# Kernel tuning notes

Hardware: AMD Instinct MI355X
Metric: run time of the kernel (lower is better)

## Reference

```python
import jax, jax.numpy as jnp
import numpy as np

T, D = 8192, 2048
EPS = 1e-5


def _layernorm(x, g, b):
    mu = jnp.mean(x, axis=-1, keepdims=True)
    var = jnp.var(x, axis=-1, keepdims=True)
    return (x - mu) * jax.lax.rsqrt(var + EPS) * g + b


def setup_inputs() -> dict:
    key = jax.random.key(0)
    ks = jax.random.split(key, 8)
    s = 0.02
    return {
        "x": jax.random.normal(ks[0], (T, D), dtype=jnp.float32),
        "ln1_g": jnp.ones((D,), jnp.float32),
        "ln1_b": jnp.zeros((D,), jnp.float32),
        "W_in": s * jax.random.normal(ks[1], (D, D), jnp.float32),
        "b_in": jnp.zeros((D,), jnp.float32),
        "W_gate": s * jax.random.normal(ks[2], (D, D), jnp.float32),
        "b_gate": jnp.zeros((D,), jnp.float32),
        "W_out": s * jax.random.normal(ks[3], (D, D), jnp.float32),
        "b_out": jnp.zeros((D,), jnp.float32),
        "state_decay": jnp.zeros((D,), jnp.float32),
        "ln2_g": jnp.ones((D,), jnp.float32),
        "ln2_b": jnp.zeros((D,), jnp.float32),
        "W_ff1": s * jax.random.normal(ks[4], (D, 2 * D), jnp.float32),
        "b_ff1": jnp.zeros((2 * D,), jnp.float32),
        "W_ff2": s * jax.random.normal(ks[5], (2 * D, D), jnp.float32),
        "b_ff2": jnp.zeros((D,), jnp.float32),
    }


def reference(x, ln1_g, ln1_b, W_in, b_in, W_gate, b_gate, W_out, b_out,
              state_decay, ln2_g, ln2_b, W_ff1, b_ff1, W_ff2, b_ff2):
    hidden = _layernorm(x, ln1_g, ln1_b)          # [T, D]
    u = hidden @ W_in + b_in                      # [T, D]
    gate = jax.nn.sigmoid(hidden @ W_gate + b_gate)
    decay = jax.nn.sigmoid(state_decay)           # [D], constant per channel

    def step(state, inp):
        u_t, g_t = inp
        state = decay * state + u_t               # diagonal linear recurrence
        return state, state * g_t

    _, state_out = jax.lax.scan(step, jnp.zeros((D,), x.dtype), (u, gate))
    x = x + state_out @ W_out + b_out
    h2 = _layernorm(x, ln2_g, ln2_b)
    ff = jax.nn.silu(h2 @ W_ff1 + b_ff1) @ W_ff2 + b_ff2
    return x + ff
```

## Files before the change

### kernel.cpp

```cpp
#include <hip/hip_runtime.h>
#include <stdint.h>

#define T_DIM 8192
#define D_DIM 2048
#define SCAN_L 128
#define SCAN_C 64

#define SH_I8 (6.0f / 127.0f)
#define SW_I8 (0.11f / 127.0f)

typedef __attribute__((ext_vector_type(8))) __bf16 bf16x8;
typedef __attribute__((ext_vector_type(4))) float f32x4;
typedef __attribute__((ext_vector_type(4))) float f4v;
typedef __attribute__((ext_vector_type(4))) unsigned short us16x4;
typedef __attribute__((ext_vector_type(4))) int i32x4;

__device__ __forceinline__ unsigned short f2bf(float f) {
  union { float f; uint32_t u; } c{f};
  uint32_t u = c.u;
  return (unsigned short)((u + 0x7FFFu + ((u >> 16) & 1u)) >> 16);
}
__device__ __forceinline__ float bf2f(unsigned short h) {
  union { uint32_t u; float f; } c{((uint32_t)h) << 16};
  return c.f;
}
__device__ __forceinline__ float sigmoidf_(float z) {
  return 1.0f / (1.0f + __expf(-z));
}
__device__ __forceinline__ int q_i8(float v, float inv_s) {
  float q = rintf(v * inv_s);
  q = fmaxf(-127.0f, fminf(127.0f, q));
  return (int)q;
}
__device__ __forceinline__ uint32_t pk4_i8(float a, float b, float c, float d,
                                           float inv_s) {
  return ((uint32_t)(q_i8(a, inv_s) & 0xFF)) |
         ((uint32_t)(q_i8(b, inv_s) & 0xFF) << 8) |
         ((uint32_t)(q_i8(c, inv_s) & 0xFF) << 16) |
         ((uint32_t)(q_i8(d, inv_s) & 0xFF) << 24);
}

__global__ void transpose_cvt(const float* __restrict__ W,
                              unsigned short* __restrict__ WT,
                              int K, int N) {
  __shared__ float tile[32][33];
  int n0 = blockIdx.x * 32, k0 = blockIdx.y * 32;
  int tx = threadIdx.x, ty = threadIdx.y;
#pragma unroll
  for (int i = 0; i < 4; ++i)
    tile[ty + i * 8][tx] = W[(size_t)(k0 + ty + i * 8) * N + n0 + tx];
  __syncthreads();
#pragma unroll
  for (int i = 0; i < 4; ++i)
    WT[(size_t)(n0 + ty + i * 8) * K + k0 + tx] = f2bf(tile[tx][ty + i * 8]);
}

__global__ void transpose_cvt_i8(const float* __restrict__ W,
                                 signed char* __restrict__ WT,
                                 int K, int N) {
  __shared__ float tile[32][33];
  int n0 = blockIdx.x * 32, k0 = blockIdx.y * 32;
  int tx = threadIdx.x, ty = threadIdx.y;
#pragma unroll
  for (int i = 0; i < 4; ++i)
    tile[ty + i * 8][tx] = W[(size_t)(k0 + ty + i * 8) * N + n0 + tx];
  __syncthreads();
  const float inv_s = 1.0f / SW_I8;
#pragma unroll
  for (int i = 0; i < 4; ++i)
    WT[(size_t)(n0 + ty + i * 8) * K + k0 + tx] =
        (signed char)q_i8(tile[tx][ty + i * 8], inv_s);
}

__global__ __launch_bounds__(256) void ln_kernel(const float* __restrict__ x,
                                                 const float* __restrict__ g,
                                                 const float* __restrict__ b,
                                                 unsigned short* __restrict__ out) {
  const int D = D_DIM;
  size_t base = (size_t)blockIdx.x * D;
  int tid = threadIdx.x;
  const f4v* xv = reinterpret_cast<const f4v*>(x + base);
  f4v v0 = xv[tid];
  f4v v1 = xv[tid + 256];
  float sum = 0.f, sq = 0.f;
#pragma unroll
  for (int i = 0; i < 4; ++i) {
    sum += v0[i] + v1[i];
    sq += v0[i] * v0[i] + v1[i] * v1[i];
  }
#pragma unroll
  for (int o = 32; o > 0; o >>= 1) {
    sum += __shfl_xor(sum, o);
    sq += __shfl_xor(sq, o);
  }
  __shared__ float red[2][4];
  int wave = tid >> 6, lane = tid & 63;
  if (lane == 0) { red[0][wave] = sum; red[1][wave] = sq; }
  __syncthreads();
  sum = red[0][0] + red[0][1] + red[0][2] + red[0][3];
  sq  = red[1][0] + red[1][1] + red[1][2] + red[1][3];
  float mu = sum * (1.0f / D);
  float rstd = rsqrtf(sq * (1.0f / D) - mu * mu + 1e-5f);
  const f4v* gv = reinterpret_cast<const f4v*>(g);
  const f4v* bv = reinterpret_cast<const f4v*>(b);
  f4v g0 = gv[tid], g1 = gv[tid + 256], b0 = bv[tid], b1 = bv[tid + 256];
  us16x4 o0, o1;
#pragma unroll
  for (int i = 0; i < 4; ++i) {
    o0[i] = f2bf((v0[i] - mu) * rstd * g0[i] + b0[i]);
    o1[i] = f2bf((v1[i] - mu) * rstd * g1[i] + b1[i]);
  }
  us16x4* ov = reinterpret_cast<us16x4*>(out + base);
  ov[tid] = o0;
  ov[tid + 256] = o1;
}

__global__ __launch_bounds__(256) void ln_kernel_i8(const float* __restrict__ x,
                                                    const float* __restrict__ g,
                                                    const float* __restrict__ b,
                                                    uint32_t* __restrict__ out) {
  const int D = D_DIM;
  size_t base = (size_t)blockIdx.x * D;
  int tid = threadIdx.x;
  const f4v* xv = reinterpret_cast<const f4v*>(x + base);
  f4v v0 = xv[tid];
  f4v v1 = xv[tid + 256];
  float sum = 0.f, sq = 0.f;
#pragma unroll
  for (int i = 0; i < 4; ++i) {
    sum += v0[i] + v1[i];
    sq += v0[i] * v0[i] + v1[i] * v1[i];
  }
#pragma unroll
  for (int o = 32; o > 0; o >>= 1) {
    sum += __shfl_xor(sum, o);
    sq += __shfl_xor(sq, o);
  }
  __shared__ float red[2][4];
  int wave = tid >> 6, lane = tid & 63;
  if (lane == 0) { red[0][wave] = sum; red[1][wave] = sq; }
  __syncthreads();
  sum = red[0][0] + red[0][1] + red[0][2] + red[0][3];
  sq  = red[1][0] + red[1][1] + red[1][2] + red[1][3];
  float mu = sum * (1.0f / D);
  float rstd = rsqrtf(sq * (1.0f / D) - mu * mu + 1e-5f);
  const f4v* gv = reinterpret_cast<const f4v*>(g);
  const f4v* bv = reinterpret_cast<const f4v*>(b);
  f4v g0 = gv[tid], g1 = gv[tid + 256], b0 = bv[tid], b1 = bv[tid + 256];
  const float inv_s = 1.0f / SH_I8;
  uint32_t* ov = out + (base >> 2);
  ov[tid] = pk4_i8((v0[0] - mu) * rstd * g0[0] + b0[0],
                   (v0[1] - mu) * rstd * g0[1] + b0[1],
                   (v0[2] - mu) * rstd * g0[2] + b0[2],
                   (v0[3] - mu) * rstd * g0[3] + b0[3], inv_s);
  ov[tid + 256] = pk4_i8((v1[0] - mu) * rstd * g1[0] + b1[0],
                         (v1[1] - mu) * rstd * g1[1] + b1[1],
                         (v1[2] - mu) * rstd * g1[2] + b1[2],
                         (v1[3] - mu) * rstd * g1[3] + b1[3], inv_s);
}

__global__ void scan_p1(const unsigned short* __restrict__ u,
                        const float* __restrict__ sdec,
                        float* __restrict__ carry) {
  int d = blockIdx.y * 256 + threadIdx.x;
  int c = blockIdx.x;
  float dec = sigmoidf_(sdec[d]);
  const unsigned short* up = u + (size_t)c * SCAN_L * D_DIM + d;
  float s = 0.f;
#pragma unroll 4
  for (int t = 0; t < SCAN_L; ++t)
    s = fmaf(dec, s, bf2f(up[(size_t)t * D_DIM]));
  carry[c * D_DIM + d] = s;
}

__global__ void scan_p2(const float* __restrict__ carry,
                        const float* __restrict__ sdec,
                        float* __restrict__ init) {
  int d = blockIdx.x * 256 + threadIdx.x;
  float dec = sigmoidf_(sdec[d]);
  float dL = dec;
#pragma unroll
  for (int i = 0; i < 7; ++i) dL *= dL;
  float s = 0.f;
  for (int c = 0; c < SCAN_C; ++c) {
    init[c * D_DIM + d] = s;
    s = fmaf(dL, s, carry[c * D_DIM + d]);
  }
}

__global__ void scan_p3(const unsigned short* __restrict__ u,
                        const unsigned short* __restrict__ gate,
                        const float* __restrict__ init,
                        const float* __restrict__ sdec,
                        unsigned short* __restrict__ stout) {
  int d = blockIdx.y * 256 + threadIdx.x;
  int c = blockIdx.x;
  float dec = sigmoidf_(sdec[d]);
  size_t off = (size_t)c * SCAN_L * D_DIM + d;
  float s = init[c * D_DIM + d];
#pragma unroll 4
  for (int t = 0; t < SCAN_L; ++t) {
    size_t o = off + (size_t)t * D_DIM;
    s = fmaf(dec, s, bf2f(u[o]));
    stout[o] = f2bf(s * bf2f(gate[o]));
  }
}

#define BARRIER() asm volatile("s_barrier" ::: "memory")
#define VM6C()    asm volatile("s_waitcnt vmcnt(6)" ::: "memory")
#define VM0C()    asm volatile("s_waitcnt vmcnt(0)" ::: "memory")
#define PRIO1()   __builtin_amdgcn_s_setprio(1)
#define PRIO0()   __builtin_amdgcn_s_setprio(0)
#define SB0()     __builtin_amdgcn_sched_barrier(0)

#define XCD_SWZ_()                                                            \
  const int gx = gridDim.x;                                                   \
  int lid = blockIdx.y * gx + blockIdx.x;                                     \
  int cpx = (gx * gridDim.y) >> 3;                                            \
  int swzid = (lid & 7) * cpx + (lid >> 3);                                   \
  int tn = swzid % gx, tm = swzid / gx;

#define MFMA_G(aSET, bSET, AH, BH)                                            \
  _Pragma("unroll") for (int m_ = 0; m_ < 4; ++m_)                            \
  _Pragma("unroll") for (int n_ = 0; n_ < 2; ++n_)                            \
  _Pragma("unroll") for (int k_ = 0; k_ < 2; ++k_)                            \
      acc[AH][BH][m_][n_] = __builtin_amdgcn_mfma_f32_16x16x32_bf16(          \
          aSET[m_][k_], bSET[n_][k_], acc[AH][BH][m_][n_], 0, 0, 0);

#define STG_(base, dst, bb, hh, kt)                                           \
  {                                                                           \
    __builtin_amdgcn_global_load_lds(                                         \
        (const __attribute__((address_space(1))) uint32_t*)((base) +          \
            (size_t)((hh) * 128) * K + (kt)),                                 \
        (__attribute__((address_space(3))) uint32_t*)((dst) +                 \
            ((bb) * 2 + (hh)) * 8192), 16, 0, 0);                             \
    __builtin_amdgcn_global_load_lds(                                         \
        (const __attribute__((address_space(1))) uint32_t*)((base) +          \
            (size_t)((hh) * 128 + 8) * K + (kt)),                             \
        (__attribute__((address_space(3))) uint32_t*)((dst) +                 \
            ((bb) * 2 + (hh)) * 8192 + 512), 16, 0, 0);                       \
  }

#define LDA_TO(dst, bb, ah)                                                   \
  {                                                                           \
    const unsigned short* p_ = As_ + ((bb) * 2 + (ah)) * 8192 + rA64;         \
    _Pragma("unroll") for (int m_ = 0; m_ < 4; ++m_) {                        \
      dst[m_][0] = *reinterpret_cast<const bf16x8*>(p_ + m_ * 1024 + sw0);    \
      dst[m_][1] = *reinterpret_cast<const bf16x8*>(p_ + m_ * 1024 + sw1);    \
    }                                                                         \
  }

#define LDB_TO(dst, bb, bh)                                                   \
  {                                                                           \
    const unsigned short* p_ = Bs_ + ((bb) * 2 + (bh)) * 8192 + rB64;         \
    _Pragma("unroll") for (int n_ = 0; n_ < 2; ++n_) {                        \
      dst[n_][0] = *reinterpret_cast<const bf16x8*>(p_ + n_ * 1024 + sw0);    \
      dst[n_][1] = *reinterpret_cast<const bf16x8*>(p_ + n_ * 1024 + sw1);    \
    }                                                                         \
  }

#define TILE_(tt, bb, B0C, B0N)                                               \
  {                                                                  \
    LDB_TO(b1, bb, 1);                                                        \
    if ((tt) + 1 < T) STG_(aS, aD, (bb) ^ 1, 1, ((tt) + 1) * 64);             \
    SB0();                                                                    \
    PRIO1(); MFMA_G(aF, B0C, 0, 0); PRIO0();                                  \
    BARRIER();                                                                \
                                                                     \
    if ((tt) + 2 < T) STG_(aS, aD, bb, 0, ((tt) + 2) * 64);                   \
    SB0();                                                                    \
    PRIO1(); MFMA_G(aF, b1, 0, 1); PRIO0();                                   \
    SB0();                                                                    \
    LDA_TO(aF, bb, 1);                                                        \
    BARRIER();                                                                \
                                                                     \
    if ((tt) + 2 < T) STG_(bS, bD, bb, 0, ((tt) + 2) * 64);                   \
    SB0();                                                                    \
    PRIO1(); MFMA_G(aF, b1, 1, 1); PRIO0();                                   \
    BARRIER();                                                                \
                                                                     \
    if ((tt) + 2 < T) STG_(bS, bD, bb, 1, ((tt) + 2) * 64);                   \
    if ((tt) < T - 2) { VM6C(); } else { VM0C(); }                            \
    BARRIER();                                                                \
    SB0();                                                                    \
    if ((tt) + 1 < T) LDB_TO(B0N, (bb) ^ 1, 0);                               \
    SB0();                                                                    \
    PRIO1(); MFMA_G(aF, B0C, 1, 0); PRIO0();                                  \
    SB0();                                                                    \
    if ((tt) + 1 < T) LDA_TO(aF, (bb) ^ 1, 0);                                \
  }

__global__ __launch_bounds__(512, 2) void gemm8(
    const unsigned short* __restrict__ A, const unsigned short* __restrict__ B,
    int M, int N, int K, const float* __restrict__ bias0,
    const float* __restrict__ res, float* __restrict__ out0) {
  extern __shared__ unsigned short lds[];
  unsigned short* As_ = lds;
  unsigned short* Bs_ = lds + 32768;

  const int tid = threadIdx.x;
  const int w = tid >> 6, l = tid & 63;
  XCD_SWZ_();
  const int mr = w >> 2, nc = w & 3;
  const int lr = l & 15, kq = l >> 4;
  const int l7 = l & 7;
  const int srow = w * 16 + (l >> 3);
  const int csl8 = ((l & 7) ^ (l >> 3)) * 8;
  const unsigned short* aS = A + (size_t)(tm * 256 + srow) * K + csl8;
  const unsigned short* bS = B + (size_t)(tn * 256 + srow) * K + csl8;
  unsigned short* aD = As_ + w * 1024 + l * 8;
  unsigned short* bD = Bs_ + w * 1024 + l * 8;
  const int rA64 = (mr * 64 + lr) * 64;
  const int rB64 = (nc * 32 + lr) * 64;
  const int sw0 = (kq ^ l7) * 8;
  const int sw1 = ((4 + kq) ^ l7) * 8;

  f32x4 acc[2][2][4][2] = {};
  bf16x8 aF[4][2], b1[2][2], b0A[2][2], b0B[2][2];
  const int T = K >> 6;

  STG_(aS, aD, 0, 0, 0);
  STG_(bS, bD, 0, 0, 0);
  STG_(bS, bD, 0, 1, 0);
  STG_(aS, aD, 0, 1, 0);
  SB0();
  STG_(aS, aD, 1, 0, 64);
  STG_(bS, bD, 1, 0, 64);
  STG_(bS, bD, 1, 1, 64);
  VM6C();
  BARRIER();
  SB0();
  LDA_TO(aF, 0, 0);
  LDB_TO(b0A, 0, 0);

  for (int t2 = 0; t2 < T; t2 += 2) {
    TILE_(t2, 0, b0A, b0B);
    TILE_(t2 + 1, 1, b0B, b0A);
  }

#pragma unroll
  for (int AH = 0; AH < 2; ++AH)
#pragma unroll
    for (int BH = 0; BH < 2; ++BH)
#pragma unroll
      for (int n = 0; n < 2; ++n) {
        int gc = tn * 256 + BH * 128 + nc * 32 + n * 16 + lr;
        float bz = bias0[gc];
#pragma unroll
        for (int m = 0; m < 4; ++m)
#pragma unroll
          for (int j = 0; j < 4; ++j) {
            int gr = tm * 256 + AH * 128 + mr * 64 + m * 16 + kq * 4 + j;
            size_t idx = (size_t)gr * N + gc;
            out0[idx] = res[idx] + acc[AH][BH][m][n][j] + bz;
          }
      }
}

#define MFMAI_(aSET, bSET, AH, BH)                                            \
  _Pragma("unroll") for (int m_ = 0; m_ < 4; ++m_)                            \
  _Pragma("unroll") for (int n_ = 0; n_ < 2; ++n_)                            \
  _Pragma("unroll") for (int k_ = 0; k_ < 2; ++k_)                            \
      acc[AH][BH][m_][n_] = __builtin_amdgcn_mfma_i32_16x16x64_i8(            \
          aSET[m_][k_], bSET[n_][k_], acc[AH][BH][m_][n_], 0, 0, 0);

#define STGX_(base, dst, bb, hh, kt)                                          \
  {                                                                           \
    __builtin_amdgcn_global_load_lds(                                         \
        (const __attribute__((address_space(1))) uint32_t*)((base) +          \
            (size_t)((hh) * 128) * K + (kt)),                                 \
        (__attribute__((address_space(3))) uint32_t*)((dst) +                 \
            ((bb) * 2 + (hh)) * 16384), 16, 0, 0);                            \
    __builtin_amdgcn_global_load_lds(                                         \
        (const __attribute__((address_space(1))) uint32_t*)((base) +          \
            (size_t)((hh) * 128 + 64) * K + (kt)),                            \
        (__attribute__((address_space(3))) uint32_t*)((dst) +                 \
            ((bb) * 2 + (hh)) * 16384 + 8192), 16, 0, 0);                     \
  }

#define LDAI_(dst, bb, ah)                                                    \
  {                                                                           \
    const signed char* p_ = As8 + ((bb) * 2 + (ah)) * 16384;                  \
    _Pragma("unroll") for (int m_ = 0; m_ < 4; ++m_) {                        \
      dst[m_][0] = *reinterpret_cast<const i32x4*>(p_ + offA0[m_]);           \
      dst[m_][1] = *reinterpret_cast<const i32x4*>(p_ + offA1[m_]);           \
    }                                                                         \
  }

#define LDBI_(dst, bb, bh)                                                    \
  {                                                                           \
    const signed char* p_ = Bs8 + ((bb) * 2 + (bh)) * 16384;                  \
    _Pragma("unroll") for (int n_ = 0; n_ < 2; ++n_) {                        \
      dst[n_][0] = *reinterpret_cast<const i32x4*>(p_ + offB0[n_]);           \
      dst[n_][1] = *reinterpret_cast<const i32x4*>(p_ + offB1[n_]);           \
    }                                                                         \
  }

#define TILEI_(tt, bb, B0C, B0N)                                              \
  {                                                                  \
    LDBI_(b1, bb, 1);                                                         \
    if ((tt) + 1 < T) STGX_(aS8, aD8, (bb) ^ 1, 1, ((tt) + 1) * 128);         \
    SB0();                                                                    \
    PRIO1(); MFMAI_(aF8, B0C, 0, 0); PRIO0();                                 \
    BARRIER();                                                                \
                                                                     \
    if ((tt) + 2 < T) STGX_(aS8, aD8, bb, 0, ((tt) + 2) * 128);               \
    SB0();                                                                    \
    PRIO1(); MFMAI_(aF8, b1, 0, 1); PRIO0();                                  \
    SB0();                                                                    \
    LDAI_(aF8, bb, 1);                                                        \
    BARRIER();                                                                \
                                                                     \
    if ((tt) + 2 < T) STGX_(bS8, bD8, bb, 0, ((tt) + 2) * 128);               \
    SB0();                                                                    \
    PRIO1(); MFMAI_(aF8, b1, 1, 1); PRIO0();                                  \
    BARRIER();                                                                \
                                                                     \
    if ((tt) + 2 < T) STGX_(bS8, bD8, bb, 1, ((tt) + 2) * 128);               \
    if ((tt) < T - 2) { VM6C(); } else { VM0C(); }                            \
    BARRIER();                                                                \
    SB0();                                                                    \
    if ((tt) + 1 < T) LDBI_(B0N, (bb) ^ 1, 0);                                \
    SB0();                                                                    \
    PRIO1(); MFMAI_(aF8, B0C, 1, 0); PRIO0();                                 \
    SB0();                                                                    \
    if ((tt) + 1 < T) LDAI_(aF8, (bb) ^ 1, 0);                                \
  }

template <int EPI>
__global__ __launch_bounds__(512, 2) void gemmI8(
    const signed char* __restrict__ A, const signed char* __restrict__ B,
    int M, int N, int K, const float* __restrict__ bias0,
    const float* __restrict__ bias1,
    unsigned short* __restrict__ out0, unsigned short* __restrict__ out1) {
  extern __shared__ signed char lds8[];
  signed char* As8 = lds8;
  signed char* Bs8 = lds8 + 65536;

  const int tid = threadIdx.x;
  const int w = tid >> 6, l = tid & 63;
  XCD_SWZ_();
  const int mr = w >> 2, nc = w & 3;
  const int lr = l & 15, kq = l >> 4;

  const int srow8 = tid >> 3;
  const int csl16 = ((tid & 7) ^ ((tid >> 3) & 7)) * 16;
  const signed char* aS8 = A + (size_t)(tm * 256 + srow8) * K + csl16;
  const signed char* bS8 = B + (size_t)(tn * 256 + srow8) * K + csl16;
  signed char* aD8 = As8 + tid * 16;
  signed char* bD8 = Bs8 + tid * 16;

  int offA0[4], offA1[4], offB0[2], offB1[2];
#pragma unroll
  for (int m_ = 0; m_ < 4; ++m_) {
    int r = mr * 64 + m_ * 16 + lr;
    offA0[m_] = r * 128 + ((kq ^ (r & 7)) * 16);
    offA1[m_] = r * 128 + (((4 + kq) ^ (r & 7)) * 16);
  }
#pragma unroll
  for (int n_ = 0; n_ < 2; ++n_) {
    int r = nc * 32 + n_ * 16 + lr;
    offB0[n_] = r * 128 + ((kq ^ (r & 7)) * 16);
    offB1[n_] = r * 128 + (((4 + kq) ^ (r & 7)) * 16);
  }

  i32x4 acc[2][2][4][2] = {};
  i32x4 aF8[4][2], b1[2][2], b0A[2][2], b0B[2][2];
  const int T = K >> 7;

  STGX_(aS8, aD8, 0, 0, 0);
  STGX_(bS8, bD8, 0, 0, 0);
  STGX_(bS8, bD8, 0, 1, 0);
  STGX_(aS8, aD8, 0, 1, 0);
  SB0();
  STGX_(aS8, aD8, 1, 0, 128);
  STGX_(bS8, bD8, 1, 0, 128);
  STGX_(bS8, bD8, 1, 1, 128);
  VM6C();
  BARRIER();
  SB0();
  LDAI_(aF8, 0, 0);
  LDBI_(b0A, 0, 0);

  for (int t2 = 0; t2 < T; t2 += 2) {
    TILEI_(t2, 0, b0A, b0B);
    TILEI_(t2 + 1, 1, b0B, b0A);
  }

  const float SDQ = SH_I8 * SW_I8;
#pragma unroll
  for (int AH = 0; AH < 2; ++AH)
#pragma unroll
    for (int BH = 0; BH < 2; ++BH)
#pragma unroll
      for (int n = 0; n < 2; ++n) {
        int gc = tn * 256 + BH * 128 + nc * 32 + n * 16 + lr;
        if (EPI == 0) {
          bool isU = gc < D_DIM;
          int cc = isU ? gc : gc - D_DIM;
          float bz = isU ? bias0[cc] : bias1[cc];
#pragma unroll
          for (int m = 0; m < 4; ++m)
#pragma unroll
            for (int j = 0; j < 4; ++j) {
              int gr = tm * 256 + AH * 128 + mr * 64 + m * 16 + kq * 4 + j;
              float v = (float)acc[AH][BH][m][n][j] * SDQ + bz;
              if (isU) out0[(size_t)gr * D_DIM + cc] = f2bf(v);
              else     out1[(size_t)gr * D_DIM + cc] = f2bf(sigmoidf_(v));
            }
        } else {
          float bz = bias0[gc];
#pragma unroll
          for (int m = 0; m < 4; ++m)
#pragma unroll
            for (int j = 0; j < 4; ++j) {
              int gr = tm * 256 + AH * 128 + mr * 64 + m * 16 + kq * 4 + j;
              float z = (float)acc[AH][BH][m][n][j] * SDQ + bz;
              out0[(size_t)gr * N + gc] = f2bf(z * sigmoidf_(z));
            }
        }
      }
}

extern "C" void kernel_launch(void* const* d_in, const int* in_sizes, int n_in,
                              void* d_out, int out_size, void* d_ws,
                              size_t ws_size, hipStream_t stream) {
  const float* x      = (const float*)d_in[0];
  const float* ln1g   = (const float*)d_in[1];
  const float* ln1b   = (const float*)d_in[2];
  const float* W_in   = (const float*)d_in[3];
  const float* b_in   = (const float*)d_in[4];
  const float* W_gate = (const float*)d_in[5];
  const float* b_gate = (const float*)d_in[6];
  const float* W_out  = (const float*)d_in[7];
  const float* b_out  = (const float*)d_in[8];
  const float* sdec   = (const float*)d_in[9];
  const float* ln2g   = (const float*)d_in[10];
  const float* ln2b   = (const float*)d_in[11];
  const float* W_ff1  = (const float*)d_in[12];
  const float* b_ff1  = (const float*)d_in[13];
  const float* W_ff2  = (const float*)d_in[14];
  const float* b_ff2  = (const float*)d_in[15];
  float* out = (float*)d_out;

  char* ws = (char*)d_ws;
  signed char*    Wi8    = (signed char*)(ws + 0);
  unsigned short* WoutT  = (unsigned short*)(ws + 16777216);
  signed char*    Wff1i8 = (signed char*)(ws + 25165824);
  unsigned short* Wff2T  = (unsigned short*)(ws + 41943040);
  unsigned short* R1     = (unsigned short*)(ws + 58720256);
  unsigned short* R2     = (unsigned short*)(ws + 92274688);
  unsigned short* R3     = (unsigned short*)(ws + 125829120);
  float* carry           = (float*)(ws + 159383552);
  float* initb           = (float*)(ws + 159907840);

  signed char*    hidi8  = (signed char*)R1;
  unsigned short* ubuf   = R2;
  unsigned short* gbuf   = R3;
  unsigned short* stout  = R1;
  signed char*    h2i8   = (signed char*)R3;
  unsigned short* abuf   = R1;

  hipFuncSetAttribute(reinterpret_cast<const void*>(&gemm8),
                      hipFuncAttributeMaxDynamicSharedMemorySize, 131072);
  hipFuncSetAttribute(reinterpret_cast<const void*>(&gemmI8<0>),
                      hipFuncAttributeMaxDynamicSharedMemorySize, 131072);
  hipFuncSetAttribute(reinterpret_cast<const void*>(&gemmI8<2>),
                      hipFuncAttributeMaxDynamicSharedMemorySize, 131072);

  dim3 tb(32, 8);
  transpose_cvt_i8<<<dim3(64, 64), tb, 0, stream>>>(W_in, Wi8, 2048, 2048);
  transpose_cvt_i8<<<dim3(64, 64), tb, 0, stream>>>(W_gate, Wi8 + 2048 * 2048, 2048, 2048);
  transpose_cvt<<<dim3(64, 64), tb, 0, stream>>>(W_out, WoutT, 2048, 2048);
  transpose_cvt_i8<<<dim3(128, 64), tb, 0, stream>>>(W_ff1, Wff1i8, 2048, 4096);
  transpose_cvt<<<dim3(64, 128), tb, 0, stream>>>(W_ff2, Wff2T, 4096, 2048);

  ln_kernel_i8<<<T_DIM, 256, 0, stream>>>(x, ln1g, ln1b, (uint32_t*)hidi8);

  gemmI8<0><<<dim3(16, 32), 512, 131072, stream>>>(
      hidi8, Wi8, T_DIM, 4096, 2048, b_in, b_gate, ubuf, gbuf);

  scan_p1<<<dim3(SCAN_C, 8), 256, 0, stream>>>(ubuf, sdec, carry);
  scan_p2<<<8, 256, 0, stream>>>(carry, sdec, initb);
  scan_p3<<<dim3(SCAN_C, 8), 256, 0, stream>>>(ubuf, gbuf, initb, sdec, stout);

  gemm8<<<dim3(8, 32), 512, 131072, stream>>>(
      stout, WoutT, T_DIM, 2048, 2048, b_out, x, out);

  ln_kernel_i8<<<T_DIM, 256, 0, stream>>>(out, ln2g, ln2b, (uint32_t*)h2i8);

  gemmI8<2><<<dim3(16, 32), 512, 131072, stream>>>(
      h2i8, Wff1i8, T_DIM, 4096, 2048, b_ff1, nullptr, abuf, nullptr);

  gemm8<<<dim3(8, 32), 512, 131072, stream>>>(
      abuf, Wff2T, T_DIM, 2048, 4096, b_ff2, out, out);
}
```

Baseline: 485.9 us.

## Add smaller-tile int8 GEMM for the fused in/gate projection

Adds a new int8 GEMM kernel, gemmI8s, with a 256x128 output tile, 48KB of LDS and launch bounds of 2 blocks per CU. It replaces the 256x256-tile gemmI8<0> for the fused W_in/W_gate projection. The launch grid doubles to 32x32, which should fill the CUs better and allow two resident blocks per CU. The trade-off is that the new kernel is single-buffered with no load/compute pipelining and has less data reuse per tile. The EPI==0 epilogue branch is removed from the templated gemmI8.

```diff
diff --git a/kernel.cpp b/kernel.cpp
--- a/kernel.cpp
+++ b/kernel.cpp
@@ -495,31 +495,110 @@
 #pragma unroll
       for (int n = 0; n < 2; ++n) {
         int gc = tn * 256 + BH * 128 + nc * 32 + n * 16 + lr;
-        if (EPI == 0) {
-          bool isU = gc < D_DIM;
-          int cc = isU ? gc : gc - D_DIM;
-          float bz = isU ? bias0[cc] : bias1[cc];
-#pragma unroll
-          for (int m = 0; m < 4; ++m)
-#pragma unroll
-            for (int j = 0; j < 4; ++j) {
-              int gr = tm * 256 + AH * 128 + mr * 64 + m * 16 + kq * 4 + j;
-              float v = (float)acc[AH][BH][m][n][j] * SDQ + bz;
-              if (isU) out0[(size_t)gr * D_DIM + cc] = f2bf(v);
-              else     out1[(size_t)gr * D_DIM + cc] = f2bf(sigmoidf_(v));
-            }
-        } else {
-          float bz = bias0[gc];
-#pragma unroll
-          for (int m = 0; m < 4; ++m)
-#pragma unroll
-            for (int j = 0; j < 4; ++j) {
-              int gr = tm * 256 + AH * 128 + mr * 64 + m * 16 + kq * 4 + j;
-              float z = (float)acc[AH][BH][m][n][j] * SDQ + bz;
-              out0[(size_t)gr * N + gc] = f2bf(z * sigmoidf_(z));
-            }
-        }
+        float bz = bias0[gc];
+#pragma unroll
+        for (int m = 0; m < 4; ++m)
+#pragma unroll
+          for (int j = 0; j < 4; ++j) {
+            int gr = tm * 256 + AH * 128 + mr * 64 + m * 16 + kq * 4 + j;
+            float z = (float)acc[AH][BH][m][n][j] * SDQ + bz;
+            out0[(size_t)gr * N + gc] = f2bf(z * sigmoidf_(z));
+          }
       }
+}
+
+__global__ __launch_bounds__(512, 2) void gemmI8s(
+    const signed char* __restrict__ A, const signed char* __restrict__ B,
+    int M, int N, int K, const float* __restrict__ bias0,
+    const float* __restrict__ bias1,
+    unsigned short* __restrict__ out0, unsigned short* __restrict__ out1) {
+  extern __shared__ signed char lds8[];
+  signed char* As8 = lds8;
+  signed char* Bs8 = lds8 + 32768;
+
+  const int tid = threadIdx.x;
+  const int w = tid >> 6, l = tid & 63;
+  XCD_SWZ_();
+  const int mr = w >> 1, nc = w & 1;
+  const int lr = l & 15, kq = l >> 4;
+
+  const int srow8 = tid >> 3;
+  const int csl16 = ((tid & 7) ^ ((tid >> 3) & 7)) * 16;
+  const signed char* aS8 = A + (size_t)(tm * 256 + srow8) * K + csl16;
+  const signed char* bS8 = B + (size_t)(tn * 128 + srow8) * K + csl16;
+  signed char* aD8 = As8 + tid * 16;
+  signed char* bD8 = Bs8 + tid * 16;
+
+  int offA0[4], offA1[4], offB0[4], offB1[4];
+#pragma unroll
+  for (int m_ = 0; m_ < 4; ++m_) {
+    int r = mr * 64 + m_ * 16 + lr;
+    offA0[m_] = r * 128 + ((kq ^ (r & 7)) * 16);
+    offA1[m_] = r * 128 + (((4 + kq) ^ (r & 7)) * 16);
+  }
+#pragma unroll
+  for (int n_ = 0; n_ < 4; ++n_) {
+    int r = nc * 64 + n_ * 16 + lr;
+    offB0[n_] = r * 128 + ((kq ^ (r & 7)) * 16);
+    offB1[n_] = r * 128 + (((4 + kq) ^ (r & 7)) * 16);
+  }
+
+  i32x4 acc[4][4] = {};
+  const int T = K >> 7;
+
+  for (int t = 0; t < T; ++t) {
+#pragma unroll
+    for (int i = 0; i < 4; ++i)
+      __builtin_amdgcn_global_load_lds(
+          (const __attribute__((address_space(1))) uint32_t*)(aS8 +
+              (size_t)(i * 64) * K + t * 128),
+          (__attribute__((address_space(3))) uint32_t*)(aD8 + i * 8192),
+          16, 0, 0);
+#pragma unroll
+    for (int i = 0; i < 2; ++i)
+      __builtin_amdgcn_global_load_lds(
+          (const __attribute__((address_space(1))) uint32_t*)(bS8 +
+              (size_t)(i * 64) * K + t * 128),
+          (__attribute__((address_space(3))) uint32_t*)(bD8 + i * 8192),
+          16, 0, 0);
+    VM0C();
+    __syncthreads();
+#pragma unroll
+    for (int c = 0; c < 2; ++c) {
+      i32x4 aF[4], bF[4];
+#pragma unroll
+      for (int m_ = 0; m_ < 4; ++m_)
+        aF[m_] = *reinterpret_cast<const i32x4*>(As8 + (c ? offA1[m_] : offA0[m_]));
+#pragma unroll
+      for (int n_ = 0; n_ < 4; ++n_)
+        bF[n_] = *reinterpret_cast<const i32x4*>(Bs8 + (c ? offB1[n_] : offB0[n_]));
+#pragma unroll
+      for (int m_ = 0; m_ < 4; ++m_)
+#pragma unroll
+        for (int n_ = 0; n_ < 4; ++n_)
+          acc[m_][n_] = __builtin_amdgcn_mfma_i32_16x16x64_i8(
+              aF[m_], bF[n_], acc[m_][n_], 0, 0, 0);
+    }
+    __syncthreads();
+  }
+
+  const float SDQ = SH_I8 * SW_I8;
+#pragma unroll
+  for (int n = 0; n < 4; ++n) {
+    int gc = tn * 128 + nc * 64 + n * 16 + lr;
+    bool isU = gc < D_DIM;
+    int cc = isU ? gc : gc - D_DIM;
+    float bz = isU ? bias0[cc] : bias1[cc];
+#pragma unroll
+    for (int m = 0; m < 4; ++m)
+#pragma unroll
+      for (int j = 0; j < 4; ++j) {
+        int gr = tm * 256 + mr * 64 + m * 16 + kq * 4 + j;
+        float v = (float)acc[m][n][j] * SDQ + bz;
+        if (isU) out0[(size_t)gr * D_DIM + cc] = f2bf(v);
+        else     out1[(size_t)gr * D_DIM + cc] = f2bf(sigmoidf_(v));
+      }
+  }
 }
 
 extern "C" void kernel_launch(void* const* d_in, const int* in_sizes, int n_in,
@@ -563,10 +642,10 @@
 
   hipFuncSetAttribute(reinterpret_cast<const void*>(&gemm8),
                       hipFuncAttributeMaxDynamicSharedMemorySize, 131072);
-  hipFuncSetAttribute(reinterpret_cast<const void*>(&gemmI8<0>),
-                      hipFuncAttributeMaxDynamicSharedMemorySize, 131072);
   hipFuncSetAttribute(reinterpret_cast<const void*>(&gemmI8<2>),
                       hipFuncAttributeMaxDynamicSharedMemorySize, 131072);
+  hipFuncSetAttribute(reinterpret_cast<const void*>(&gemmI8s),
+                      hipFuncAttributeMaxDynamicSharedMemorySize, 49152);
 
   dim3 tb(32, 8);
   transpose_cvt_i8<<<dim3(64, 64), tb, 0, stream>>>(W_in, Wi8, 2048, 2048);
@@ -577,7 +656,7 @@
 
   ln_kernel_i8<<<T_DIM, 256, 0, stream>>>(x, ln1g, ln1b, (uint32_t*)hidi8);
 
-  gemmI8<0><<<dim3(16, 32), 512, 131072, stream>>>(
+  gemmI8s<<<dim3(32, 32), 512, 49152, stream>>>(
       hidi8, Wi8, T_DIM, 4096, 2048, b_in, b_gate, ubuf, gbuf);
 
   scan_p1<<<dim3(SCAN_C, 8), 256, 0, stream>>>(ubuf, sdec, carry);
```

Measured after the change: 488.3 us. About the same (+0.5%).
